# Optimization experiments

Hardware: AMD Instinct MI355X
Metric: run time of the kernel (lower is better)

Reference implementation:

```python
import jax, jax.numpy as jnp
import numpy as np
import math

D, H, L, V, F, B, S = 1024, 16, 4, 32000, 4096, 1, 2048
HD = D // H
LN_EPS = 1e-5


def _alibi_slopes(n_heads):
    # power-of-2 case from the torch code
    start = 2.0 ** (-2.0 ** (-(math.log2(n_heads) - 3)))
    return np.array([start * (start ** i) for i in range(n_heads)], dtype=np.float32)


def setup_inputs() -> dict:
    key = jax.random.key(0)
    ks = jax.random.split(key, 10)
    sc = 0.02
    return {
        "input_ids": jax.random.randint(ks[0], (B, S), 0, V, dtype=jnp.int64 if jax.config.jax_enable_x64 else jnp.int32),
        "emb": jax.random.normal(ks[1], (V, D), jnp.float32) * sc,
        "alibi_slopes": jnp.asarray(_alibi_slopes(H)),
        "Wq": jax.random.normal(ks[2], (L, D, D), jnp.float32) * sc,
        "Wk": jax.random.normal(ks[3], (L, D, D), jnp.float32) * sc,
        "Wv": jax.random.normal(ks[4], (L, D, D), jnp.float32) * sc,
        "Wo": jax.random.normal(ks[5], (L, D, D), jnp.float32) * sc,
        "W1": jax.random.normal(ks[6], (L, F, D), jnp.float32) * sc,
        "b1": jnp.zeros((L, F), jnp.float32),
        "W2": jax.random.normal(ks[7], (L, D, F), jnp.float32) * sc,
        "b2": jnp.zeros((L, D), jnp.float32),
        "g1": jnp.ones((L, D), jnp.float32),
        "beta1": jnp.zeros((L, D), jnp.float32),
        "g2": jnp.ones((L, D), jnp.float32),
        "beta2": jnp.zeros((L, D), jnp.float32),
        "gf": jnp.ones((D,), jnp.float32),
        "bf": jnp.zeros((D,), jnp.float32),
    }


def _layernorm(x, g, b):
    m = jnp.mean(x, axis=-1, keepdims=True)
    v = jnp.var(x, axis=-1, keepdims=True)
    return (x - m) * jax.lax.rsqrt(v + LN_EPS) * g + b


def _forward(input_ids, emb, alibi_slopes, Wq, Wk, Wv, Wo, W1, b1, W2, b2,
             g1, beta1, g2, beta2, gf, bf):
    x = emb[input_ids]  # [B, S, D]
    pos = jnp.arange(S, dtype=jnp.float32)
    dist = pos[None, :] - pos[:, None]          # [S, S], entry (i, j) = j - i
    causal = dist <= 0                           # tril mask
    bias = alibi_slopes[None, :, None, None] * dist  # [1, H, S, S]
    scale = 1.0 / math.sqrt(HD)

    def layer(x, p):
        wq, wk, wv, wo, w1, bb1, w2, bb2, gg1, be1, gg2, be2 = p
        h = _layernorm(x, gg1, be1)
        q = jnp.einsum('bsd,ed->bse', h, wq).reshape(B, S, H, HD).transpose(0, 2, 1, 3)
        k = jnp.einsum('bsd,ed->bse', h, wk).reshape(B, S, H, HD).transpose(0, 2, 1, 3)
        v = jnp.einsum('bsd,ed->bse', h, wv).reshape(B, S, H, HD).transpose(0, 2, 1, 3)
        scores = jnp.einsum('bhqd,bhkd->bhqk', q, k) * scale
        scores = scores - bias
        scores = jnp.where(causal, scores, -jnp.inf)
        w = jax.nn.softmax(scores, axis=-1)
        out = jnp.einsum('bhqk,bhkd->bhqd', w, v)
        out = out.transpose(0, 2, 1, 3).reshape(B, S, D)
        out = jnp.einsum('bsd,ed->bse', out, wo)
        x = x + out
        h2 = _layernorm(x, gg2, be2)
        ff = jax.nn.gelu(jnp.einsum('bsd,fd->bsf', h2, w1) + bb1, approximate=False)
        ff = jnp.einsum('bsf,df->bsd', ff, w2) + bb2
        return x + ff, None

    params = (Wq, Wk, Wv, Wo, W1, b1, W2, b2, g1, beta1, g2, beta2)
    x, _ = jax.lax.scan(layer, x, params)
    x = _layernorm(x, gf, bf)
    logits = jnp.einsum('bsd,vd->bsv', x, emb)  # tied lm_head
    return logits


def reference(input_ids, emb, alibi_slopes, Wq, Wk, Wv, Wo, W1, b1, W2, b2,
              g1, beta1, g2, beta2, gf, bf):
    return _forward(input_ids, emb, alibi_slopes, Wq, Wk, Wv, Wo, W1, b1, W2, b2,
                    g1, beta1, g2, beta2, gf, bf)
```

## Files before the change

### kernel.cpp

```cpp
#include <hip/hip_runtime.h>
#include <hip/hip_bf16.h>

typedef unsigned int u32;
typedef unsigned short u16;
typedef __attribute__((ext_vector_type(8))) __bf16 bf16x8;
typedef __attribute__((ext_vector_type(8))) unsigned short u16x8;
typedef __attribute__((ext_vector_type(4))) float f32x4;

#define SEQ 2048

__device__ __forceinline__ float b2f(u16 u) {
  union { u32 i; float f; } x; x.i = ((u32)u) << 16; return x.f;
}
__device__ __forceinline__ u16 f2b(float f) {
  u32 u = __float_as_uint(f);
  u = (u + 0x7fffu + ((u >> 16) & 1u)) >> 16;
  return (u16)u;
}
__device__ __forceinline__ void gload_lds16(const void* g, void* l) {
  __builtin_amdgcn_global_load_lds((const __attribute__((address_space(1))) u32*)g,
                                   (__attribute__((address_space(3))) u32*)l, 16, 0, 0);
}

struct CvtArgs {
  const float* src[7];
  u16* dst[7];
  u32 beg[8];
  u32 total;
};

__global__ __launch_bounds__(256) void cvt_all(CvtArgs a)
{
  for (u32 i = blockIdx.x * 256 + threadIdx.x; i < a.total; i += gridDim.x * 256) {
    int s = 0;
#pragma unroll
    for (int k = 1; k < 7; ++k) s += (i >= a.beg[k]);
    const u32 li = i - a.beg[s];
    const float* in = a.src[s];
    const float4 f0 = ((const float4*)in)[(size_t)li * 2];
    const float4 f1 = ((const float4*)in)[(size_t)li * 2 + 1];
    union { bf16x8 b; u16x8 u; } r;
    r.b[0] = (__bf16)f0.x; r.b[1] = (__bf16)f0.y;
    r.b[2] = (__bf16)f0.z; r.b[3] = (__bf16)f0.w;
    r.b[4] = (__bf16)f1.x; r.b[5] = (__bf16)f1.y;
    r.b[6] = (__bf16)f1.z; r.b[7] = (__bf16)f1.w;
    *(u16x8*)(a.dst[s] + (size_t)li * 8) = r.u;
  }
}

__global__ __launch_bounds__(512, 2) void gemm256(
    const u16* __restrict__ A, const u16* __restrict__ Bt,
    float* __restrict__ C, int N, int K)
{
  __shared__ u16 As[2][256 * 64];
  __shared__ u16 Bs[2][256 * 64];
  const int tid = threadIdx.x;
  const int lane = tid & 63;
  const int wid = tid >> 6;
  const int wr = wid >> 2;
  const int wc = wid & 3;

  const int T = (int)gridDim.x;
  const int bid = (int)blockIdx.x;
  const int q8 = T >> 3, r8 = T & 7;
  const int xcd = bid & 7, base = bid >> 3;
  const int swz = (xcd < r8 ? xcd * (q8 + 1) : r8 * (q8 + 1) + (xcd - r8) * q8) + base;
  const int m0 = (swz & 7) * 256;
  const int n0 = (swz >> 3) * 256;

  f32x4 acc[8][4] = {};

  const int srow = tid >> 3;
  const int sgr = (tid & 7) ^ (srow & 7);
  const u16* gA = A + (size_t)(m0 + srow) * K + sgr * 8;
  const u16* gB = Bt + (size_t)(n0 + srow) * K + sgr * 8;
  const int dwave = wid * 512;

  const int co0 = (((lane >> 4)) ^ (lane & 7)) * 8;
  const int co1 = (((lane >> 4) + 4) ^ (lane & 7)) * 8;
  const int raA = (wr * 128 + (lane & 15)) * 64;
  const int raB = (wc * 64 + (lane & 15)) * 64;

#pragma unroll
  for (int c = 0; c < 4; ++c) {
    gload_lds16(gA + (size_t)(c * 64) * K, &As[0][c * 4096 + dwave]);
    gload_lds16(gB + (size_t)(c * 64) * K, &Bs[0][c * 4096 + dwave]);
  }
  asm volatile("s_waitcnt vmcnt(0)" ::: "memory");
  __syncthreads();

  const int nk = K >> 6;
#pragma unroll 2
  for (int t = 0; t < nk; ++t) {
    const int cb = t & 1;
    const int sb = cb ^ 1;
    const u16* Acur = &As[cb][0];
    const u16* Bcur = &Bs[cb][0];
    u16* Anxt = &As[sb][0];
    u16* Bnxt = &Bs[sb][0];
    const size_t ktn = (size_t)(t + 1) * 64;
    const bool stg = (t + 1 < nk);
    bf16x8 bf[4][2];
#pragma unroll
    for (int p = 0; p < 4; ++p) {
      bf16x8 af[2][2];
#pragma unroll
      for (int mm = 0; mm < 2; ++mm) {
        const int ro = raA + (p * 32 + mm * 16) * 64;
        af[mm][0] = *(const bf16x8*)&Acur[ro + co0];
        af[mm][1] = *(const bf16x8*)&Acur[ro + co1];
      }
      if (p == 0) {
#pragma unroll
        for (int n = 0; n < 4; ++n) {
          const int ro = raB + n * 16 * 64;
          bf[n][0] = *(const bf16x8*)&Bcur[ro + co0];
          bf[n][1] = *(const bf16x8*)&Bcur[ro + co1];
        }
      }
      if (stg) {
        if (p < 2) {
          gload_lds16(gA + (size_t)((p * 2 + 0) * 64) * K + ktn, Anxt + (p * 2 + 0) * 4096 + dwave);
          gload_lds16(gA + (size_t)((p * 2 + 1) * 64) * K + ktn, Anxt + (p * 2 + 1) * 4096 + dwave);
        } else {
          gload_lds16(gB + (size_t)(((p - 2) * 2 + 0) * 64) * K + ktn, Bnxt + ((p - 2) * 2 + 0) * 4096 + dwave);
          gload_lds16(gB + (size_t)(((p - 2) * 2 + 1) * 64) * K + ktn, Bnxt + ((p - 2) * 2 + 1) * 4096 + dwave);
        }
      }
      __syncthreads();
      __builtin_amdgcn_s_setprio(1);
#pragma unroll
      for (int mm = 0; mm < 2; ++mm)
#pragma unroll
        for (int n = 0; n < 4; ++n) {
          acc[p * 2 + mm][n] = __builtin_amdgcn_mfma_f32_16x16x32_bf16(af[mm][0], bf[n][0], acc[p * 2 + mm][n], 0, 0, 0);
          acc[p * 2 + mm][n] = __builtin_amdgcn_mfma_f32_16x16x32_bf16(af[mm][1], bf[n][1], acc[p * 2 + mm][n], 0, 0, 0);
        }
      __builtin_amdgcn_s_setprio(0);
      if (p == 3) asm volatile("s_waitcnt vmcnt(0)" ::: "memory");
      __syncthreads();
    }
  }

  const int crow = m0 + wr * 128 + ((lane >> 4) << 2);
  const int ccol = n0 + wc * 64 + (lane & 15);
#pragma unroll
  for (int m = 0; m < 8; ++m)
#pragma unroll
    for (int n = 0; n < 4; ++n)
#pragma unroll
      for (int j = 0; j < 4; ++j)
        C[(size_t)(crow + m * 16 + j) * N + ccol + n * 16] = acc[m][n][j];
}

template <int EPI>
__global__ __launch_bounds__(256) void gemm64(
    const u16* __restrict__ A, const u16* __restrict__ B0,
    const u16* __restrict__ B1, const u16* __restrict__ B2,
    void* __restrict__ C0, void* __restrict__ C1, void* __restrict__ C2,
    const float* __restrict__ bias, int N, int K)
{
  __shared__ u16 As[64 * 64];
  __shared__ u16 Bs[128 * 64];
  const int tid = threadIdx.x;
  const int lane = tid & 63;
  const int w = tid >> 6;
  const int wr = w >> 1;
  const int wc = w & 1;

  const int T = (int)gridDim.x;
  const int bid = (int)blockIdx.x;
  const int q8 = T >> 3, r8 = T & 7;
  const int xcd = bid & 7, base = bid >> 3;
  int swz = (xcd < r8 ? xcd * (q8 + 1) : r8 * (q8 + 1) + (xcd - r8) * q8) + base;
  int which = 0;
  if (EPI == 1) which = swz >> 8;
  const u16* Bt = (which == 0) ? B0 : (which == 1) ? B1 : B2;
  const int m0 = (swz & 31) * 64;
  const int n0 = (EPI == 1 ? ((swz >> 5) & 7) : (swz >> 5)) * 128;

  const int kchunk = K / (int)gridDim.z;
  const int kbeg = (int)blockIdx.z * kchunk;
  const int kend = kbeg + kchunk;

  f32x4 acc[2][4] = {};

  const int rs = lane >> 3;
  const int gs = (lane & 7) ^ rs;
  const u16* ga0 = A + (size_t)(m0 + w * 16 + rs) * K + gs * 8;
  const u16* gb0 = Bt + (size_t)(n0 + w * 32 + rs) * K + gs * 8;
  u16* la = &As[(w * 16) * 64];
  u16* lb = &Bs[(w * 32) * 64];

  const int xg = lane & 7;
  int coff[2];
#pragma unroll
  for (int ks = 0; ks < 2; ++ks)
    coff[ks] = ((ks * 4 + (lane >> 4)) ^ xg) * 8;
  const int ra = (wr * 32 + (lane & 15)) * 64;
  const int rb = (wc * 64 + (lane & 15)) * 64;

  for (int kt = kbeg; kt < kend; kt += 64) {
    __syncthreads();
#pragma unroll
    for (int c = 0; c < 2; ++c)
      gload_lds16(ga0 + (size_t)c * 8 * K + kt, la + c * 8 * 64);
#pragma unroll
    for (int c = 0; c < 4; ++c)
      gload_lds16(gb0 + (size_t)c * 8 * K + kt, lb + c * 8 * 64);
    asm volatile("s_waitcnt vmcnt(0)" ::: "memory");
    __syncthreads();
#pragma unroll
    for (int ks = 0; ks < 2; ++ks) {
      bf16x8 af[2], bfr[4];
#pragma unroll
      for (int m = 0; m < 2; ++m)
        af[m] = *(const bf16x8*)&As[ra + m * 16 * 64 + coff[ks]];
#pragma unroll
      for (int n = 0; n < 4; ++n)
        bfr[n] = *(const bf16x8*)&Bs[rb + n * 16 * 64 + coff[ks]];
#pragma unroll
      for (int m = 0; m < 2; ++m)
#pragma unroll
        for (int n = 0; n < 4; ++n)
          acc[m][n] = __builtin_amdgcn_mfma_f32_16x16x32_bf16(af[m], bfr[n], acc[m][n], 0, 0, 0);
    }
  }

#pragma unroll
  for (int m = 0; m < 2; ++m) {
    const int rowb = m0 + wr * 32 + m * 16 + ((lane >> 4) << 2);
#pragma unroll
    for (int n = 0; n < 4; ++n) {
      const int col = n0 + wc * 64 + n * 16 + (lane & 15);
#pragma unroll
      for (int j = 0; j < 4; ++j) {
        const int r = rowb + j;
        float v = acc[m][n][j];
        if (EPI == 1) {
          u16* outp = (u16*)((which == 0) ? C0 : (which == 1) ? C1 : C2);
          outp[((size_t)(col >> 6) * SEQ + r) * 64 + (col & 63)] = f2b(v);
        } else if (EPI == 2) {
          float xx = v + bias[col];
          float ge = 0.5f * xx * (1.0f + erff(xx * 0.70710678118654752f));
          ((u16*)C0)[(size_t)r * N + col] = f2b(ge);
        } else {
          float xx = v;
          if (bias != nullptr && blockIdx.z == 0) xx += bias[col];
          atomicAdd(&((float*)C0)[(size_t)r * N + col], xx);
        }
      }
    }
  }
}

__global__ __launch_bounds__(256) void gemm_f32b(
    const u16* __restrict__ A, const float* __restrict__ Bt,
    float* __restrict__ C0, int N, int K)
{
  __shared__ u16 As[128 * 32];
  __shared__ u16 Bs[128 * 32];
  const int tid = threadIdx.x;
  const int lane = tid & 63;
  const int w = tid >> 6;
  const int wr = w >> 1;
  const int wc = w & 1;

  const int T = (int)gridDim.x;
  const int bid = (int)blockIdx.x;
  const int q8 = T >> 3, r8 = T & 7;
  const int xcd = bid & 7, base = bid >> 3;
  int swz = (xcd < r8 ? xcd * (q8 + 1) : r8 * (q8 + 1) + (xcd - r8) * q8) + base;
  const int m0 = (swz & 15) * 128;
  const int n0 = (swz >> 4) * 128;

  f32x4 acc[4][4] = {};
  const u16* ga0 = A + (size_t)(m0 + w * 32 + (lane >> 2)) * K + (lane & 3) * 8;
  u16* la = &As[(w * 32) * 32];
  const float* gb32 = Bt + (size_t)(n0 + (tid >> 1)) * K + (tid & 1) * 16;
  u16* lbw = &Bs[(tid >> 1) * 32 + (tid & 1) * 16];

  for (int kt = 0; kt < K; kt += 32) {
    __syncthreads();
    gload_lds16(ga0 + kt, la);
    gload_lds16(ga0 + kt + 16 * K, la + 16 * 32);
    {
      const float4 f0 = *(const float4*)(gb32 + kt);
      const float4 f1 = *(const float4*)(gb32 + kt + 4);
      const float4 f2 = *(const float4*)(gb32 + kt + 8);
      const float4 f3 = *(const float4*)(gb32 + kt + 12);
      union { bf16x8 b; u16x8 u; } lo, hi;
      lo.b[0] = (__bf16)f0.x; lo.b[1] = (__bf16)f0.y;
      lo.b[2] = (__bf16)f0.z; lo.b[3] = (__bf16)f0.w;
      lo.b[4] = (__bf16)f1.x; lo.b[5] = (__bf16)f1.y;
      lo.b[6] = (__bf16)f1.z; lo.b[7] = (__bf16)f1.w;
      hi.b[0] = (__bf16)f2.x; hi.b[1] = (__bf16)f2.y;
      hi.b[2] = (__bf16)f2.z; hi.b[3] = (__bf16)f2.w;
      hi.b[4] = (__bf16)f3.x; hi.b[5] = (__bf16)f3.y;
      hi.b[6] = (__bf16)f3.z; hi.b[7] = (__bf16)f3.w;
      *(u16x8*)lbw = lo.u;
      *(u16x8*)(lbw + 8) = hi.u;
    }
    asm volatile("s_waitcnt vmcnt(0)" ::: "memory");
    __syncthreads();
    bf16x8 af[4], bfr[4];
#pragma unroll
    for (int m = 0; m < 4; ++m)
      af[m] = *(const bf16x8*)&As[(wr * 64 + m * 16 + (lane & 15)) * 32 + (lane >> 4) * 8];
#pragma unroll
    for (int n = 0; n < 4; ++n)
      bfr[n] = *(const bf16x8*)&Bs[(wc * 64 + n * 16 + (lane & 15)) * 32 + (lane >> 4) * 8];
#pragma unroll
    for (int m = 0; m < 4; ++m)
#pragma unroll
      for (int n = 0; n < 4; ++n)
        acc[m][n] = __builtin_amdgcn_mfma_f32_16x16x32_bf16(af[m], bfr[n], acc[m][n], 0, 0, 0);
  }

#pragma unroll
  for (int m = 0; m < 4; ++m) {
    const int rowb = m0 + wr * 64 + m * 16 + ((lane >> 4) << 2);
#pragma unroll
    for (int n = 0; n < 4; ++n) {
      const int col = n0 + wc * 64 + n * 16 + (lane & 15);
#pragma unroll
      for (int j = 0; j < 4; ++j)
        C0[(size_t)(rowb + j) * N + col] = acc[m][n][j];
    }
  }
}

__global__ __launch_bounds__(256) void ln_kernel(const float* __restrict__ x,
    const float* __restrict__ g, const float* __restrict__ b, u16* __restrict__ out)
{
  const int row = blockIdx.x;
  const int tid = threadIdx.x;
  const float4 v = ((const float4*)(x + (size_t)row * 1024))[tid];
  float s = v.x + v.y + v.z + v.w;
  float sq = v.x * v.x + v.y * v.y + v.z * v.z + v.w * v.w;
#pragma unroll
  for (int o = 1; o < 64; o <<= 1) { s += __shfl_xor(s, o); sq += __shfl_xor(sq, o); }
  __shared__ float ss[4], ssq[4];
  if ((tid & 63) == 0) { ss[tid >> 6] = s; ssq[tid >> 6] = sq; }
  __syncthreads();
  s = ss[0] + ss[1] + ss[2] + ss[3];
  sq = ssq[0] + ssq[1] + ssq[2] + ssq[3];
  const float mean = s * (1.0f / 1024.0f);
  const float var = sq * (1.0f / 1024.0f) - mean * mean;
  const float rstd = rsqrtf(var + 1e-5f);
  const int c = tid * 4;
  u16* o4 = out + (size_t)row * 1024 + c;
  const float4 gg = ((const float4*)g)[tid];
  const float4 bb = ((const float4*)b)[tid];
  o4[0] = f2b((v.x - mean) * rstd * gg.x + bb.x);
  o4[1] = f2b((v.y - mean) * rstd * gg.y + bb.y);
  o4[2] = f2b((v.z - mean) * rstd * gg.z + bb.z);
  o4[3] = f2b((v.w - mean) * rstd * gg.w + bb.w);
}

__global__ __launch_bounds__(256) void gather_kernel(const int* __restrict__ ids,
    const float* __restrict__ emb, float* __restrict__ x)
{
  const int srow = blockIdx.x;
  const int tid = threadIdx.x;
  const int id = ids[srow];
  ((float4*)(x + (size_t)srow * 1024))[tid] =
      ((const float4*)(emb + (size_t)id * 1024))[tid];
}

__global__ __launch_bounds__(256) void attn_kernel(
    const u16* __restrict__ q, const u16* __restrict__ k, const u16* __restrict__ v,
    const float* __restrict__ slopes, u16* __restrict__ out)
{
  const int bid = (int)blockIdx.x;
  const int swz = (bid & 7) * 32 + (bid >> 3);
  const int h = swz >> 4;
  const int q0 = (swz & 15) * 128;
  const int tid = threadIdx.x;
  const int lane = tid & 63;
  const int w = tid >> 6;
  const float slope = slopes[h];

  __shared__ u16 Ks[2][64 * 32];
  __shared__ u16 Vt[64][72];
  __shared__ u16 Pl[4][32][72];

  const u16* qb = q + ((size_t)h * SEQ + q0 + w * 32) * 64;
  bf16x8 qf[2][2];
#pragma unroll
  for (int m = 0; m < 2; ++m)
#pragma unroll
    for (int kk = 0; kk < 2; ++kk)
      qf[m][kk] = *(const bf16x8*)(qb + (m * 16 + (lane & 15)) * 64 + kk * 32 + (lane >> 4) * 8);

  f32x4 o_acc[2][4] = {};
  float mrun[2][4], lrun[2][4];
#pragma unroll
  for (int m = 0; m < 2; ++m)
#pragma unroll
    for (int j = 0; j < 4; ++j) { mrun[m][j] = -1e30f; lrun[m][j] = 0.0f; }

  const int ntiles = (q0 >> 6) + 2;
  const int wmaxrow = q0 + w * 32 + 31;

  const int kkp = w >> 1, halfp = w & 1;
  const u16* gk0 = k + ((size_t)h * SEQ + halfp * 32 + (lane >> 2)) * 64 + kkp * 32 + (lane & 3) * 8;
  u16* lk = &Ks[kkp][(halfp * 32) * 32];
  const u16* gv0 = v + ((size_t)h * SEQ + lane) * 64 + w * 16;

  for (int t = 0; t < ntiles; ++t) {
    const int j0 = t << 6;
    __syncthreads();
    gload_lds16(gk0 + (size_t)j0 * 64, lk);
    gload_lds16(gk0 + (size_t)(j0 + 16) * 64, lk + 16 * 32);
    {
      const u16* gvp = gv0 + (size_t)j0 * 64;
      u16x8 v0 = *(const u16x8*)gvp;
      u16x8 v1 = *(const u16x8*)(gvp + 8);
      const int d0 = w * 16;
#pragma unroll
      for (int i = 0; i < 8; ++i) Vt[d0 + i][lane] = v0[i];
#pragma unroll
      for (int i = 0; i < 8; ++i) Vt[d0 + 8 + i][lane] = v1[i];
    }
    asm volatile("s_waitcnt vmcnt(0)" ::: "memory");
    __syncthreads();

    if (wmaxrow >= j0) {
      f32x4 s[2][4] = {};
      __builtin_amdgcn_s_setprio(1);
#pragma unroll
      for (int kk = 0; kk < 2; ++kk) {
        bf16x8 kf[4];
#pragma unroll
        for (int n = 0; n < 4; ++n)
          kf[n] = *(const bf16x8*)&Ks[kk][(n * 16 + (lane & 15)) * 32 + (lane >> 4) * 8];
#pragma unroll
        for (int m = 0; m < 2; ++m)
#pragma unroll
          for (int n = 0; n < 4; ++n)
            s[m][n] = __builtin_amdgcn_mfma_f32_16x16x32_bf16(qf[m][kk], kf[n], s[m][n], 0, 0, 0);
      }
      __builtin_amdgcn_s_setprio(0);
      const int rq = q0 + w * 32 + ((lane >> 4) << 2);
      const int ck = j0 + (lane & 15);
#pragma unroll
      for (int m = 0; m < 2; ++m) {
#pragma unroll
        for (int j = 0; j < 4; ++j) {
          const int qi = rq + m * 16 + j;
          float mx = -1e30f;
#pragma unroll
          for (int n = 0; n < 4; ++n) {
            const int kj = ck + n * 16;
            float val = s[m][n][j] * 0.125f - slope * (float)(kj - qi);
            val = (kj <= qi) ? val : -1e30f;
            s[m][n][j] = val;
            mx = fmaxf(mx, val);
          }
#pragma unroll
          for (int o = 1; o < 16; o <<= 1) mx = fmaxf(mx, __shfl_xor(mx, o));
          const float mnew = fmaxf(mrun[m][j], mx);
          const float alpha = __expf(mrun[m][j] - mnew);
          mrun[m][j] = mnew;
          float rs = 0.0f;
          const int prow = m * 16 + ((lane >> 4) << 2) + j;
#pragma unroll
          for (int n = 0; n < 4; ++n) {
            const float p = __expf(s[m][n][j] - mnew);
            rs += p;
            Pl[w][prow][n * 16 + (lane & 15)] = f2b(p);
          }
#pragma unroll
          for (int o = 1; o < 16; o <<= 1) rs += __shfl_xor(rs, o);
          lrun[m][j] = lrun[m][j] * alpha + rs;
#pragma unroll
          for (int n = 0; n < 4; ++n) o_acc[m][n][j] *= alpha;
        }
      }
      __builtin_amdgcn_s_setprio(1);
#pragma unroll
      for (int kk = 0; kk < 2; ++kk) {
        bf16x8 pf[2], vf[4];
#pragma unroll
        for (int m = 0; m < 2; ++m)
          pf[m] = *(const bf16x8*)&Pl[w][m * 16 + (lane & 15)][kk * 32 + (lane >> 4) * 8];
#pragma unroll
        for (int n = 0; n < 4; ++n)
          vf[n] = *(const bf16x8*)&Vt[n * 16 + (lane & 15)][kk * 32 + (lane >> 4) * 8];
#pragma unroll
        for (int m = 0; m < 2; ++m)
#pragma unroll
          for (int n = 0; n < 4; ++n)
            o_acc[m][n] = __builtin_amdgcn_mfma_f32_16x16x32_bf16(pf[m], vf[n], o_acc[m][n], 0, 0, 0);
      }
      __builtin_amdgcn_s_setprio(0);
    }
  }

#pragma unroll
  for (int m = 0; m < 2; ++m) {
    const int sbase = q0 + w * 32 + m * 16 + ((lane >> 4) << 2);
#pragma unroll
    for (int n = 0; n < 4; ++n) {
      const int d = h * 64 + n * 16 + (lane & 15);
#pragma unroll
      for (int j = 0; j < 4; ++j)
        out[(size_t)(sbase + j) * 1024 + d] = f2b(o_acc[m][n][j] / lrun[m][j]);
    }
  }
}

extern "C" void kernel_launch(void* const* d_in, const int* in_sizes, int n_in,
                              void* d_out, int out_size, void* d_ws, size_t ws_size,
                              hipStream_t stream)
{
  (void)in_sizes; (void)n_in; (void)out_size;
  const int* ids = (const int*)d_in[0];
  const float* emb = (const float*)d_in[1];
  const float* slopes = (const float*)d_in[2];
  const float* Wq = (const float*)d_in[3];
  const float* Wk = (const float*)d_in[4];
  const float* Wv = (const float*)d_in[5];
  const float* Wo = (const float*)d_in[6];
  const float* W1 = (const float*)d_in[7];
  const float* b1 = (const float*)d_in[8];
  const float* W2 = (const float*)d_in[9];
  const float* b2 = (const float*)d_in[10];
  const float* g1 = (const float*)d_in[11];
  const float* be1 = (const float*)d_in[12];
  const float* g2 = (const float*)d_in[13];
  const float* be2 = (const float*)d_in[14];
  const float* gf = (const float*)d_in[15];
  const float* bfin = (const float*)d_in[16];

  char* ob = (char*)d_out;
  float* x   = (float*)ob;
  u16* qb    = (u16*)(ob + (size_t)( 8u << 20));
  u16* kb    = (u16*)(ob + (size_t)(12u << 20));
  u16* vb    = (u16*)(ob + (size_t)(16u << 20));
  u16* attn  = (u16*)(ob + (size_t)(20u << 20));
  u16* ff    = (u16*)(ob + (size_t)(24u << 20));
  u16* Wq_b  = (u16*)(ob + (size_t)( 40u << 20));
  u16* Wk_b  = (u16*)(ob + (size_t)( 48u << 20));
  u16* Wv_b  = (u16*)(ob + (size_t)( 56u << 20));
  u16* Wo_b  = (u16*)(ob + (size_t)( 64u << 20));
  u16* W1_b  = (u16*)(ob + (size_t)( 72u << 20));
  u16* W2_b  = (u16*)(ob + (size_t)(104u << 20));
  u16* h     = (u16*)d_ws;
  const size_t emb_b_need = (size_t)(4u << 20) + (size_t)32000 * 1024 * 2;
  const bool emb_fits = ws_size >= emb_b_need;
  u16* emb_b = (u16*)((char*)d_ws + (4u << 20));
  float* logits = (float*)d_out;

  {
    CvtArgs a;
    const u32 wsz = 4 * 1024 * 1024 / 8;
    const u32 fsz = 16 * 1024 * 1024 / 8;
    const u32 esz = 32000 * 1024 / 8;
    a.src[0] = Wq; a.dst[0] = Wq_b;
    a.src[1] = Wk; a.dst[1] = Wk_b;
    a.src[2] = Wv; a.dst[2] = Wv_b;
    a.src[3] = Wo; a.dst[3] = Wo_b;
    a.src[4] = W1; a.dst[4] = W1_b;
    a.src[5] = W2; a.dst[5] = W2_b;
    a.src[6] = emb; a.dst[6] = emb_b;
    a.beg[0] = 0;
    a.beg[1] = wsz;      a.beg[2] = 2 * wsz;  a.beg[3] = 3 * wsz;
    a.beg[4] = 4 * wsz;  a.beg[5] = 4 * wsz + fsz;  a.beg[6] = 4 * wsz + 2 * fsz;
    a.beg[7] = a.beg[6] + esz;
    a.total = emb_fits ? a.beg[7] : a.beg[6];
    cvt_all<<<2048, 256, 0, stream>>>(a);
  }

  gather_kernel<<<2048, 256, 0, stream>>>(ids, emb, x);

  for (int l = 0; l < 4; ++l) {
    const size_t wo = (size_t)l * 1024 * 1024;
    const size_t wf = (size_t)l * 4096 * 1024;
    ln_kernel<<<2048, 256, 0, stream>>>(x, g1 + l * 1024, be1 + l * 1024, h);
    gemm64<1><<<dim3(768, 1, 1), 256, 0, stream>>>(h, Wq_b + wo, Wk_b + wo, Wv_b + wo,
        qb, kb, vb, nullptr, 1024, 1024);
    attn_kernel<<<dim3(256, 1, 1), 256, 0, stream>>>(qb, kb, vb, slopes, attn);
    gemm64<3><<<dim3(256, 1, 2), 256, 0, stream>>>(attn, Wo_b + wo, nullptr, nullptr,
        x, nullptr, nullptr, nullptr, 1024, 1024);
    ln_kernel<<<2048, 256, 0, stream>>>(x, g2 + l * 1024, be2 + l * 1024, h);
    gemm64<2><<<dim3(1024, 1, 1), 256, 0, stream>>>(h, W1_b + wf, nullptr, nullptr,
        ff, nullptr, nullptr, b1 + l * 4096, 4096, 1024);
    gemm64<3><<<dim3(256, 1, 2), 256, 0, stream>>>(ff, W2_b + wf, nullptr, nullptr,
        x, nullptr, nullptr, b2 + l * 1024, 1024, 4096);
  }
  ln_kernel<<<2048, 256, 0, stream>>>(x, gf, bfin, h);
  if (emb_fits) {
    gemm256<<<dim3(1000, 1, 1), 512, 0, stream>>>(h, emb_b, logits, 32000, 1024);
  } else {
    gemm_f32b<<<dim3(4000, 1, 1), 256, 0, stream>>>(h, emb, logits, 32000, 1024);
  }
}
```

Measured before the change: 1.385 ms.

## Prefetch two K-tiles ahead in 256x256 GEMM and cut per-phase barriers

The large-tile GEMM now issues the global-to-LDS loads for both the first and second K-tiles up front. In steady state it refills the just-consumed buffer with tile t+2 after each K-step, waiting with vmcnt(8) so the next tile's loads stay in flight. The eight barriers per K-step (two per sub-phase) become two per K-step, and all B fragments are read at the top of the step. This hides more global latency and removes sync overhead, but the LDS buffer reuse now depends on the exact vmcnt counting and barrier placement being right.

```diff
diff --git a/kernel.cpp b/kernel.cpp
--- a/kernel.cpp
+++ b/kernel.cpp
@@ -81,26 +81,35 @@
   const int raA = (wr * 128 + (lane & 15)) * 64;
   const int raB = (wc * 64 + (lane & 15)) * 64;
 
+  const int nk = K >> 6;
+
 #pragma unroll
   for (int c = 0; c < 4; ++c) {
     gload_lds16(gA + (size_t)(c * 64) * K, &As[0][c * 4096 + dwave]);
     gload_lds16(gB + (size_t)(c * 64) * K, &Bs[0][c * 4096 + dwave]);
   }
-  asm volatile("s_waitcnt vmcnt(0)" ::: "memory");
-  __syncthreads();
-
-  const int nk = K >> 6;
+#pragma unroll
+  for (int c = 0; c < 4; ++c) {
+    gload_lds16(gA + (size_t)(c * 64) * K + 64, &As[1][c * 4096 + dwave]);
+    gload_lds16(gB + (size_t)(c * 64) * K + 64, &Bs[1][c * 4096 + dwave]);
+  }
+  asm volatile("s_waitcnt vmcnt(8)" ::: "memory");
+  __builtin_amdgcn_s_barrier();
+  __builtin_amdgcn_sched_barrier(0);
+
 #pragma unroll 2
   for (int t = 0; t < nk; ++t) {
     const int cb = t & 1;
-    const int sb = cb ^ 1;
     const u16* Acur = &As[cb][0];
     const u16* Bcur = &Bs[cb][0];
-    u16* Anxt = &As[sb][0];
-    u16* Bnxt = &Bs[sb][0];
-    const size_t ktn = (size_t)(t + 1) * 64;
-    const bool stg = (t + 1 < nk);
+
     bf16x8 bf[4][2];
+#pragma unroll
+    for (int n = 0; n < 4; ++n) {
+      const int ro = raB + n * 16 * 64;
+      bf[n][0] = *(const bf16x8*)&Bcur[ro + co0];
+      bf[n][1] = *(const bf16x8*)&Bcur[ro + co1];
+    }
 #pragma unroll
     for (int p = 0; p < 4; ++p) {
       bf16x8 af[2][2];
@@ -110,24 +119,6 @@
         af[mm][0] = *(const bf16x8*)&Acur[ro + co0];
         af[mm][1] = *(const bf16x8*)&Acur[ro + co1];
       }
-      if (p == 0) {
-#pragma unroll
-        for (int n = 0; n < 4; ++n) {
-          const int ro = raB + n * 16 * 64;
-          bf[n][0] = *(const bf16x8*)&Bcur[ro + co0];
-          bf[n][1] = *(const bf16x8*)&Bcur[ro + co1];
-        }
-      }
-      if (stg) {
-        if (p < 2) {
-          gload_lds16(gA + (size_t)((p * 2 + 0) * 64) * K + ktn, Anxt + (p * 2 + 0) * 4096 + dwave);
-          gload_lds16(gA + (size_t)((p * 2 + 1) * 64) * K + ktn, Anxt + (p * 2 + 1) * 4096 + dwave);
-        } else {
-          gload_lds16(gB + (size_t)(((p - 2) * 2 + 0) * 64) * K + ktn, Bnxt + ((p - 2) * 2 + 0) * 4096 + dwave);
-          gload_lds16(gB + (size_t)(((p - 2) * 2 + 1) * 64) * K + ktn, Bnxt + ((p - 2) * 2 + 1) * 4096 + dwave);
-        }
-      }
-      __syncthreads();
       __builtin_amdgcn_s_setprio(1);
 #pragma unroll
       for (int mm = 0; mm < 2; ++mm)
@@ -137,9 +128,24 @@
           acc[p * 2 + mm][n] = __builtin_amdgcn_mfma_f32_16x16x32_bf16(af[mm][1], bf[n][1], acc[p * 2 + mm][n], 0, 0, 0);
         }
       __builtin_amdgcn_s_setprio(0);
-      if (p == 3) asm volatile("s_waitcnt vmcnt(0)" ::: "memory");
-      __syncthreads();
-    }
+    }
+
+    __builtin_amdgcn_s_barrier();
+    if (t + 2 < nk) {
+      const size_t kto = (size_t)(t + 2) * 64;
+      u16* Anx = &As[cb][0];
+      u16* Bnx = &Bs[cb][0];
+#pragma unroll
+      for (int c = 0; c < 4; ++c) {
+        gload_lds16(gA + (size_t)(c * 64) * K + kto, Anx + c * 4096 + dwave);
+        gload_lds16(gB + (size_t)(c * 64) * K + kto, Bnx + c * 4096 + dwave);
+      }
+      asm volatile("s_waitcnt vmcnt(8)" ::: "memory");
+    } else if (t + 1 < nk) {
+      asm volatile("s_waitcnt vmcnt(0)" ::: "memory");
+    }
+    __builtin_amdgcn_s_barrier();
+    __builtin_amdgcn_sched_barrier(0);
   }
 
   const int crow = m0 + wr * 128 + ((lane >> 4) << 2);
```

New measurement: 1.319 ms. 4.8% less time.
